# Kernel tuning notes

Hardware: AMD Instinct MI355X
Metric: run time of the kernel (lower is better)

The kernel has to match this reference:

```python
import jax, jax.numpy as jnp
import numpy as np

D_MODEL = 1024
N_HEADS = 16
D_HEAD = D_MODEL // N_HEADS
B, L = 4, 2048


def setup_inputs() -> dict:
    key = jax.random.key(0)
    ks = jax.random.split(key, 10)
    s = 1.0 / np.sqrt(D_MODEL)
    inp = {
        "x": jax.random.normal(ks[0], (B, L, D_MODEL), dtype=jnp.float32),
        "src_key_padding_mask": jax.random.randint(ks[1], (B, L), 0, 2) > 0,
        "wq": jax.random.uniform(ks[2], (D_MODEL, D_MODEL), jnp.float32, -s, s),
        "bq": jnp.zeros((D_MODEL,), jnp.float32),
        "wk": jax.random.uniform(ks[3], (D_MODEL, D_MODEL), jnp.float32, -s, s),
        "bk": jnp.zeros((D_MODEL,), jnp.float32),
        "wv": jax.random.uniform(ks[4], (D_MODEL, D_MODEL), jnp.float32, -s, s),
        "bv": jnp.zeros((D_MODEL,), jnp.float32),
        "wo": jax.random.uniform(ks[5], (D_MODEL, D_MODEL), jnp.float32, -s, s),
        "bo": jnp.zeros((D_MODEL,), jnp.float32),
    }
    return inp


def reference(x, src_key_padding_mask, wq, bq, wk, bk, wv, bv, wo, bo):
    # dropout is identity in eval mode
    Bx, Lx, D = x.shape
    H, dh = N_HEADS, D_HEAD

    def proj(w, b):
        # torch nn.Linear: y = x @ w.T + b
        y = jnp.einsum('bld,ed->ble', x, w) + b
        return y.reshape(Bx, Lx, H, dh).transpose(0, 2, 1, 3)  # (B,H,L,dh)

    q = proj(wq, bq)
    k = proj(wk, bk)
    v = proj(wv, bv)

    scores = jnp.einsum('bhqd,bhkd->bhqk', q, k) / jnp.sqrt(jnp.float32(dh))
    scores = jnp.where(src_key_padding_mask[:, None, None, :], jnp.float32(-1e9), scores)
    attn = jax.nn.softmax(scores, axis=-1)
    out = jnp.einsum('bhqk,bhkd->bhqd', attn, v)
    out = out.transpose(0, 2, 1, 3).reshape(Bx, Lx, D)
    out = jnp.einsum('bld,ed->ble', out, wo) + bo
    return out
```

## Files before the change

### kernel.cpp

```cpp
#include <hip/hip_runtime.h>


typedef __attribute__((ext_vector_type(8))) short short8;
typedef __attribute__((ext_vector_type(4))) float f32x4;
typedef __attribute__((ext_vector_type(4))) float floatx4;
typedef __attribute__((ext_vector_type(4))) int int4v;
typedef __attribute__((ext_vector_type(2))) unsigned int u32x2;

#define MFMA16(a, b, c) __builtin_amdgcn_mfma_f32_16x16x32_bf16((a), (b), (c), 0, 0, 0)

__device__ __forceinline__ short f2bf(float f) {
    unsigned u = __float_as_uint(f);
    u += 0x7FFF + ((u >> 16) & 1);
    return (short)(u >> 16);
}

__device__ __forceinline__ void gload_lds16(const short* g, short* l) {
    __builtin_amdgcn_global_load_lds(
        (const __attribute__((address_space(1))) void*)g,
        (__attribute__((address_space(3))) void*)l, 16, 0, 0);
}

__device__ __forceinline__ void cvt8(const float* __restrict__ src,
                                     short* __restrict__ dst, int i) {
    const f32x4* p = (const f32x4*)src + (size_t)i * 2;
    const f32x4 u0 = p[0];
    const f32x4 u1 = p[1];
    short8 s;
    s[0] = f2bf(u0[0]); s[1] = f2bf(u0[1]); s[2] = f2bf(u0[2]); s[3] = f2bf(u0[3]);
    s[4] = f2bf(u1[0]); s[5] = f2bf(u1[1]); s[6] = f2bf(u1[2]); s[7] = f2bf(u1[3]);
    ((short8*)dst)[i] = s;
}

__global__ __launch_bounds__(256) void cvt_kernel(
    const float* __restrict__ src, short* __restrict__ dst, int n8)
{
    const int i = blockIdx.x * 256 + threadIdx.x;
    if (i >= n8) return;
    cvt8(src, dst, i);
}

__global__ __launch_bounds__(256) void cvt3_kernel(
    const float* __restrict__ s0, const float* __restrict__ s1,
    const float* __restrict__ s2, short* __restrict__ d0,
    short* __restrict__ d1, short* __restrict__ d2)
{
    const int which = blockIdx.x >> 9;
    const int i = (blockIdx.x & 511) * 256 + threadIdx.x;
    const float* s = which == 0 ? s0 : which == 1 ? s1 : s2;
    short* d = which == 0 ? d0 : which == 1 ? d1 : d2;
    cvt8(s, d, i);
}

__global__ __launch_bounds__(256) void cvt2_kernel(
    const float* __restrict__ s0, short* __restrict__ d0,
    const float* __restrict__ s1, short* __restrict__ d1)
{
    if (blockIdx.x < 4096) {
        cvt8(s0, d0, blockIdx.x * 256 + threadIdx.x);
    } else {
        cvt8(s1, d1, (blockIdx.x - 4096) * 256 + threadIdx.x);
    }
}

__device__ __forceinline__ void gemm_body(
    const short* __restrict__ A, const short* __restrict__ W,
    const float* __restrict__ bias, void* __restrict__ out,
    int layout, int m0, int n0)
{
    __shared__ short As[128 * 32];
    __shared__ short Bs[128 * 32];

    const int t = threadIdx.x;
    const int wave = t >> 6, lane = t & 63;
    const int wm = (wave >> 1) * 64, wn = (wave & 1) * 64;
    const int l15 = lane & 15, quad = lane >> 4;

    const int r4 = lane >> 2;
    const int kc = (lane & 3) * 8;

    short* lA0 = &As[wave * 512 + lane * 8];
    short* lA1 = &As[2048 + wave * 512 + lane * 8];
    short* lB0 = &Bs[wave * 512 + lane * 8];
    short* lB1 = &Bs[2048 + wave * 512 + lane * 8];

    const short* gA0 = A + (size_t)(m0 + wave * 16 + r4) * 1024 + kc;
    const short* gA1 = gA0 + (size_t)64 * 1024;
    const short* gB0 = W + (size_t)(n0 + wave * 16 + r4) * 1024 + kc;
    const short* gB1 = gB0 + (size_t)64 * 1024;

    floatx4 acc[4][4];
#pragma unroll
    for (int i = 0; i < 4; i++)
#pragma unroll
        for (int j = 0; j < 4; j++) {
            acc[i][j][0] = 0.f; acc[i][j][1] = 0.f;
            acc[i][j][2] = 0.f; acc[i][j][3] = 0.f;
        }

    for (int kb = 0; kb < 1024; kb += 32) {
        gload_lds16(gA0 + kb, lA0);
        gload_lds16(gA1 + kb, lA1);
        gload_lds16(gB0 + kb, lB0);
        gload_lds16(gB1 + kb, lB1);
        __syncthreads();

        short8 af[4], bfr[4];
#pragma unroll
        for (int mi = 0; mi < 4; mi++)
            af[mi] = *(short8*)&As[(wm + mi * 16 + l15) * 32 + quad * 8];
#pragma unroll
        for (int ni = 0; ni < 4; ni++)
            bfr[ni] = *(short8*)&Bs[(wn + ni * 16 + l15) * 32 + quad * 8];
#pragma unroll
        for (int mi = 0; mi < 4; mi++)
#pragma unroll
            for (int ni = 0; ni < 4; ni++)
                acc[mi][ni] = MFMA16(af[mi], bfr[ni], acc[mi][ni]);

        __syncthreads();
    }

#pragma unroll
    for (int ni = 0; ni < 4; ni++) {
        const int gn = n0 + wn + ni * 16 + l15;
        const float bv = bias[gn];
#pragma unroll
        for (int mi = 0; mi < 4; mi++) {
#pragma unroll
            for (int r = 0; r < 4; r++) {
                const int gm = m0 + wm + mi * 16 + quad * 4 + r;
                const float v = acc[mi][ni][r] + bv;
                if (layout == 3) {
                    ((float*)out)[(size_t)gm * 1024 + gn] = v;
                } else {
                    const int b = gm >> 11, l = gm & 2047;
                    const int h = gn >> 6,  d = gn & 63;
                    size_t idx;
                    if (layout == 2)
                        idx = ((size_t)(b * 16 + h) * 64 + d) * 2048 + l;
                    else
                        idx = ((size_t)(b * 16 + h) * 2048 + l) * 64 + d;
                    ((short*)out)[idx] = f2bf(v);
                }
            }
        }
    }
}

__global__ __launch_bounds__(256, 3) void qkv_kernel(
    const short* __restrict__ Xb,
    const short* __restrict__ Wq, const short* __restrict__ Wk,
    const short* __restrict__ Wv,
    const float* __restrict__ bq, const float* __restrict__ bk,
    const float* __restrict__ bv,
    short* __restrict__ Qo, short* __restrict__ Ko, short* __restrict__ Vo)
{
    const int chunk = blockIdx.y >> 3;
    const int n0 = (blockIdx.y & 7) * 128;
    const short* W = chunk == 0 ? Wq : chunk == 1 ? Wk : Wv;
    const float* bs = chunk == 0 ? bq : chunk == 1 ? bk : bv;
    void* out = chunk == 0 ? (void*)Qo : chunk == 1 ? (void*)Ko : (void*)Vo;
    gemm_body(Xb, W, bs, out, chunk, blockIdx.x * 128, n0);
}

__global__ __launch_bounds__(256, 3) void gemm_kernel(
    const short* __restrict__ A, const short* __restrict__ W,
    const float* __restrict__ bias, void* __restrict__ out, int layout)
{
    gemm_body(A, W, bias, out, layout, blockIdx.x * 128, blockIdx.y * 128);
}

__global__ __launch_bounds__(256, 2) void attn_kernel(
    const short* __restrict__ Q, const short* __restrict__ Kc,
    const short* __restrict__ VT, const int* __restrict__ mask,
    float* __restrict__ O)
{
    __shared__ short Plds_all[4][4][16 * 72];

    const int blk = blockIdx.x;
    const int bh = blk & 63;
    const int qg = blk >> 6;
    const int b = bh >> 4, h = bh & 15;
    const int t = threadIdx.x;
    const int wave = t >> 6, lane = t & 63;
    const int l15 = lane & 15, quad = lane >> 4;

    const short* Qb = Q  + (size_t)bh * 2048 * 64;
    const short* Kb = Kc + (size_t)bh * 2048 * 64;
    const short* Vb = VT + (size_t)bh * 64 * 2048;
    const int* mrow = mask + b * 2048;

    const float SC = 0.125f * 1.44269504f;

    const int qbase = qg * 256 + wave * 64;

    short8 aq[4][2];
#pragma unroll
    for (int tt = 0; tt < 4; tt++) {
        const short* qp = Qb + (size_t)(qbase + tt * 16 + l15) * 64 + quad * 8;
        aq[tt][0] = *(const short8*)(qp);
        aq[tt][1] = *(const short8*)(qp + 32);
    }

    short8 vone;
#pragma unroll
    for (int j = 0; j < 8; j++) vone[j] = (short)0x3F80;

    floatx4 accO[4][5];
#pragma unroll
    for (int tt = 0; tt < 4; tt++)
#pragma unroll
        for (int ni = 0; ni < 5; ni++) {
            accO[tt][ni][0] = 0.f; accO[tt][ni][1] = 0.f;
            accO[tt][ni][2] = 0.f; accO[tt][ni][3] = 0.f;
        }

    for (int c0 = 0; c0 < 2048; c0 += 64) {
        short8 kreg[4][2];
#pragma unroll
        for (int g = 0; g < 4; g++) {
            const short* kp = Kb + (size_t)(c0 + g * 16 + l15) * 64 + quad * 8;
            kreg[g][0] = *(const short8*)(kp);
            kreg[g][1] = *(const short8*)(kp + 32);
        }
        f32x4 bias[4];
#pragma unroll
        for (int g = 0; g < 4; g++) {
            const int4v mv = *(const int4v*)&mrow[c0 + g * 16 + quad * 4];
#pragma unroll
            for (int r = 0; r < 4; r++) bias[g][r] = mv[r] ? -1e9f : 0.f;
        }
        short8 vreg[4][2];
#pragma unroll
        for (int ni = 0; ni < 4; ni++) {
            const short* vp = Vb + (size_t)(ni * 16 + l15) * 2048 + c0 + quad * 8;
            vreg[ni][0] = *(const short8*)(vp);
            vreg[ni][1] = *(const short8*)(vp + 32);
        }

#pragma unroll
        for (int tt = 0; tt < 4; tt++) {
            floatx4 s[4];
            __builtin_amdgcn_s_setprio(1);
#pragma unroll
            for (int g = 0; g < 4; g++) {
                floatx4 z = bias[g];
                z = MFMA16(kreg[g][0], aq[tt][0], z);
                s[g] = MFMA16(kreg[g][1], aq[tt][1], z);
            }
            __builtin_amdgcn_s_setprio(0);
            short* Pl = &Plds_all[wave][tt][0];
#pragma unroll
            for (int g = 0; g < 4; g++) {
                const float p0 = exp2f(s[g][0] * SC);
                const float p1 = exp2f(s[g][1] * SC);
                const float p2 = exp2f(s[g][2] * SC);
                const float p3 = exp2f(s[g][3] * SC);
                unsigned lo, hi;
                asm("v_cvt_pk_bf16_f32 %0, %1, %2" : "=v"(lo) : "v"(p0), "v"(p1));
                asm("v_cvt_pk_bf16_f32 %0, %1, %2" : "=v"(hi) : "v"(p2), "v"(p3));
                u32x2 w; w[0] = lo; w[1] = hi;
                *(u32x2*)&Pl[l15 * 72 + g * 16 + quad * 4] = w;
            }
        }

        asm volatile("s_waitcnt lgkmcnt(0)" ::: "memory");

#pragma unroll
        for (int tt = 0; tt < 4; tt++) {
            const short* Pl = &Plds_all[wave][tt][0];
            const short8 pa0 = *(const short8*)&Pl[l15 * 72 + quad * 8];
            const short8 pa1 = *(const short8*)&Pl[l15 * 72 + 32 + quad * 8];
            __builtin_amdgcn_s_setprio(1);
#pragma unroll
            for (int ni = 0; ni < 4; ni++) {
                accO[tt][ni] = MFMA16(pa0, vreg[ni][0], accO[tt][ni]);
                accO[tt][ni] = MFMA16(pa1, vreg[ni][1], accO[tt][ni]);
            }
            accO[tt][4] = MFMA16(pa0, vone, accO[tt][4]);
            accO[tt][4] = MFMA16(pa1, vone, accO[tt][4]);
            __builtin_amdgcn_s_setprio(0);
        }
    }

#pragma unroll
    for (int tt = 0; tt < 4; tt++) {
#pragma unroll
        for (int r = 0; r < 4; r++) {
            const float inv = 1.0f / fmaxf(accO[tt][4][r], 1e-30f);
            const int l = qbase + tt * 16 + quad * 4 + r;
#pragma unroll
            for (int ni = 0; ni < 4; ni++) {
                O[(size_t)(b * 2048 + l) * 1024 + h * 64 + ni * 16 + l15] =
                    accO[tt][ni][r] * inv;
            }
        }
    }
}

extern "C" void kernel_launch(void* const* d_in, const int* in_sizes, int n_in,
                              void* d_out, int out_size, void* d_ws, size_t ws_size,
                              hipStream_t stream)
{
    const float* x    = (const float*)d_in[0];
    const int*   mask = (const int*)d_in[1];
    const float* wq   = (const float*)d_in[2];
    const float* bq   = (const float*)d_in[3];
    const float* wk   = (const float*)d_in[4];
    const float* bk   = (const float*)d_in[5];
    const float* wv   = (const float*)d_in[6];
    const float* bv   = (const float*)d_in[7];
    const float* wo   = (const float*)d_in[8];
    const float* bo   = (const float*)d_in[9];
    float* out = (float*)d_out;

    short* Qbuf = (short*)d_ws;
    short* Kbuf = Qbuf + (size_t)8 * 1024 * 1024;
    short* Vt   = Kbuf + (size_t)8 * 1024 * 1024;

    short* Xb  = (short*)d_out;
    short* Wqb = Xb  + (size_t)8 * 1024 * 1024;
    short* Wkb = Wqb + (size_t)1024 * 1024;
    short* Wvb = Wkb + (size_t)1024 * 1024;

    dim3 block(256);

    cvt_kernel<<<dim3(4096), block, 0, stream>>>(x, Xb, 1024 * 1024);
    cvt3_kernel<<<dim3(1536), block, 0, stream>>>(wq, wk, wv, Wqb, Wkb, Wvb);

    qkv_kernel<<<dim3(64, 24), block, 0, stream>>>(
        Xb, Wqb, Wkb, Wvb, bq, bk, bv, Qbuf, Kbuf, Vt);

    attn_kernel<<<dim3(512), block, 0, stream>>>(Qbuf, Kbuf, Vt, mask, out);

    short* Ob  = Qbuf;
    short* Wob = Kbuf;
    cvt2_kernel<<<dim3(4608), block, 0, stream>>>(out, Ob, wo, Wob);

    gemm_kernel<<<dim3(64, 8), block, 0, stream>>>(Ob, Wob, bo, out, 3);
}
```

Baseline: 357.4 us.

## Use 256x256 tiled GEMMs with double-buffered LDS pipeline and tile swizzle

Replaces the 128x128 single-stage GEMM body with a 256x256 tile computed by 512 threads. It double-buffers K=64 slices in 128KB of dynamic LDS and interleaves global-to-LDS staging with MFMA phases, using explicit waitcnt, barriers and setprio. Block indices are remapped so neighbouring blocks share operand rows, which should help L2 reuse. The larger tile raises data reuse per load, but it leaves the output projection with only 128 blocks and the QKV GEMM with 384 blocks. That may underfill the CUs and give poor wave balance.

Measured after the change: 421.4 us. 17.9% more time.

```diff
diff --git a/kernel.cpp b/kernel.cpp
--- a/kernel.cpp
+++ b/kernel.cpp
@@ -63,73 +63,110 @@
     }
 }
 
-__device__ __forceinline__ void gemm_body(
+__device__ __forceinline__ void gemm256_body(
     const short* __restrict__ A, const short* __restrict__ W,
     const float* __restrict__ bias, void* __restrict__ out,
-    int layout, int m0, int n0)
-{
-    __shared__ short As[128 * 32];
-    __shared__ short Bs[128 * 32];
-
+    int layout, int m0, int n0, short* lds)
+{
     const int t = threadIdx.x;
     const int wave = t >> 6, lane = t & 63;
-    const int wm = (wave >> 1) * 64, wn = (wave & 1) * 64;
+    const int wr = wave >> 2, wc = wave & 3;
     const int l15 = lane & 15, quad = lane >> 4;
 
-    const int r4 = lane >> 2;
-    const int kc = (lane & 3) * 8;
-
-    short* lA0 = &As[wave * 512 + lane * 8];
-    short* lA1 = &As[2048 + wave * 512 + lane * 8];
-    short* lB0 = &Bs[wave * 512 + lane * 8];
-    short* lB1 = &Bs[2048 + wave * 512 + lane * 8];
-
-    const short* gA0 = A + (size_t)(m0 + wave * 16 + r4) * 1024 + kc;
-    const short* gA1 = gA0 + (size_t)64 * 1024;
-    const short* gB0 = W + (size_t)(n0 + wave * 16 + r4) * 1024 + kc;
-    const short* gB1 = gB0 + (size_t)64 * 1024;
-
-    floatx4 acc[4][4];
-#pragma unroll
-    for (int i = 0; i < 4; i++)
+    const int grow = t >> 3;
+    const int gcol = (t & 7) * 8;
+    const short* gA = A + (size_t)(m0 + grow) * 1024 + gcol;
+    const short* gB = W + (size_t)(n0 + grow) * 1024 + gcol;
+    short* ldst = lds + t * 8;
+
+    const int arow = (wr * 128 + l15) * 64 + quad * 8;
+    const int brow = 16384 + (wc * 64 + l15) * 64 + quad * 8;
+
+    f32x4 acc[8][4];
+#pragma unroll
+    for (int i = 0; i < 8; i++)
 #pragma unroll
         for (int j = 0; j < 4; j++) {
             acc[i][j][0] = 0.f; acc[i][j][1] = 0.f;
             acc[i][j][2] = 0.f; acc[i][j][3] = 0.f;
         }
 
-    for (int kb = 0; kb < 1024; kb += 32) {
-        gload_lds16(gA0 + kb, lA0);
-        gload_lds16(gA1 + kb, lA1);
-        gload_lds16(gB0 + kb, lB0);
-        gload_lds16(gB1 + kb, lB1);
-        __syncthreads();
-
-        short8 af[4], bfr[4];
-#pragma unroll
-        for (int mi = 0; mi < 4; mi++)
-            af[mi] = *(short8*)&As[(wm + mi * 16 + l15) * 32 + quad * 8];
-#pragma unroll
-        for (int ni = 0; ni < 4; ni++)
-            bfr[ni] = *(short8*)&Bs[(wn + ni * 16 + l15) * 32 + quad * 8];
-#pragma unroll
-        for (int mi = 0; mi < 4; mi++)
-#pragma unroll
-            for (int ni = 0; ni < 4; ni++)
-                acc[mi][ni] = MFMA16(af[mi], bfr[ni], acc[mi][ni]);
-
-        __syncthreads();
-    }
+#define STAGE(T, h, isA, p) do {                                              \
+    const short* g_ = ((isA) ? gA : gB) + (size_t)((h) * 128) * 1024          \
+                      + (size_t)(T) * 64;                                     \
+    short* l_ = ldst + (p) * 32768 + ((isA) ? 0 : 16384) + (h) * 8192;        \
+    gload_lds16(g_, l_);                                                      \
+    gload_lds16(g_ + 64 * 1024, l_ + 4096);                                   \
+} while (0)
+
+    short8 bf[4][2];
+
+#define PHASE(p, q, T_st, h_st, isA_st, p_st, do_vm) do {                     \
+    short8 af[2][2];                                                          \
+    _Pragma("unroll")                                                         \
+    for (int j = 0; j < 2; j++)                                               \
+        _Pragma("unroll")                                                     \
+        for (int ks = 0; ks < 2; ks++)                                        \
+            af[j][ks] = *(const short8*)                                      \
+                &lds[(p) * 32768 + arow + ((q) * 2 + j) * 1024 + ks * 32];    \
+    if ((q) == 0) {                                                           \
+        _Pragma("unroll")                                                     \
+        for (int ni = 0; ni < 4; ni++)                                        \
+            _Pragma("unroll")                                                 \
+            for (int ks = 0; ks < 2; ks++)                                    \
+                bf[ni][ks] = *(const short8*)                                 \
+                    &lds[(p) * 32768 + brow + ni * 1024 + ks * 32];           \
+    }                                                                         \
+    STAGE(T_st, h_st, isA_st, p_st);                                          \
+    if (do_vm) asm volatile("s_waitcnt vmcnt(4)");                            \
+    __builtin_amdgcn_s_barrier();                                             \
+    asm volatile("s_waitcnt lgkmcnt(0)");                                     \
+    __builtin_amdgcn_sched_barrier(0);                                        \
+    __builtin_amdgcn_s_setprio(1);                                            \
+    _Pragma("unroll")                                                         \
+    for (int j = 0; j < 2; j++)                                               \
+        _Pragma("unroll")                                                     \
+        for (int ni = 0; ni < 4; ni++) {                                      \
+            acc[(q) * 2 + j][ni] =                                            \
+                MFMA16(af[j][0], bf[ni][0], acc[(q) * 2 + j][ni]);            \
+            acc[(q) * 2 + j][ni] =                                            \
+                MFMA16(af[j][1], bf[ni][1], acc[(q) * 2 + j][ni]);            \
+        }                                                                     \
+    __builtin_amdgcn_s_setprio(0);                                            \
+    __builtin_amdgcn_s_barrier();                                             \
+} while (0)
+
+    STAGE(0, 0, false, 0); STAGE(0, 1, false, 0);
+    STAGE(0, 0, true,  0); STAGE(0, 1, true,  0);
+    STAGE(1, 0, false, 1); STAGE(1, 1, false, 1);
+    asm volatile("s_waitcnt vmcnt(4)");
+    __builtin_amdgcn_s_barrier();
+
+    for (int i = 0; i < 8; i++) {
+        const int t1 = 2 * i + 1;
+        const int n2 = (2 * i + 2) & 15;
+        const int n3 = (2 * i + 3) & 15;
+        PHASE(0, 0, t1, 0, true,  1, false);
+        PHASE(0, 1, t1, 1, true,  1, false);
+        PHASE(0, 2, n2, 0, false, 0, false);
+        PHASE(0, 3, n2, 1, false, 0, true);
+        PHASE(1, 0, n2, 0, true,  0, false);
+        PHASE(1, 1, n2, 1, true,  0, false);
+        PHASE(1, 2, n3, 0, false, 1, false);
+        PHASE(1, 3, n3, 1, false, 1, true);
+    }
+#undef PHASE
+#undef STAGE
 
 #pragma unroll
     for (int ni = 0; ni < 4; ni++) {
-        const int gn = n0 + wn + ni * 16 + l15;
+        const int gn = n0 + wc * 64 + ni * 16 + l15;
         const float bv = bias[gn];
 #pragma unroll
-        for (int mi = 0; mi < 4; mi++) {
+        for (int mi = 0; mi < 8; mi++) {
 #pragma unroll
             for (int r = 0; r < 4; r++) {
-                const int gm = m0 + wm + mi * 16 + quad * 4 + r;
+                const int gm = m0 + wr * 128 + mi * 16 + quad * 4 + r;
                 const float v = acc[mi][ni][r] + bv;
                 if (layout == 3) {
                     ((float*)out)[(size_t)gm * 1024 + gn] = v;
@@ -148,7 +185,7 @@
     }
 }
 
-__global__ __launch_bounds__(256, 3) void qkv_kernel(
+__global__ __launch_bounds__(512, 2) void qkv_kernel(
     const short* __restrict__ Xb,
     const short* __restrict__ Wq, const short* __restrict__ Wk,
     const short* __restrict__ Wv,
@@ -156,19 +193,27 @@
     const float* __restrict__ bv,
     short* __restrict__ Qo, short* __restrict__ Ko, short* __restrict__ Vo)
 {
-    const int chunk = blockIdx.y >> 3;
-    const int n0 = (blockIdx.y & 7) * 128;
+    extern __shared__ short lds[];
+    const int id = blockIdx.y * 32 + blockIdx.x;
+    const int nid = (id & 7) * 48 + (id >> 3);
+    const int bx = nid & 31, by = nid >> 5;
+    const int chunk = by >> 2;
+    const int n0 = (by & 3) * 256;
     const short* W = chunk == 0 ? Wq : chunk == 1 ? Wk : Wv;
     const float* bs = chunk == 0 ? bq : chunk == 1 ? bk : bv;
     void* out = chunk == 0 ? (void*)Qo : chunk == 1 ? (void*)Ko : (void*)Vo;
-    gemm_body(Xb, W, bs, out, chunk, blockIdx.x * 128, n0);
-}
-
-__global__ __launch_bounds__(256, 3) void gemm_kernel(
+    gemm256_body(Xb, W, bs, out, chunk, bx * 256, n0, lds);
+}
+
+__global__ __launch_bounds__(512, 2) void gemm_kernel(
     const short* __restrict__ A, const short* __restrict__ W,
     const float* __restrict__ bias, void* __restrict__ out, int layout)
 {
-    gemm_body(A, W, bias, out, layout, blockIdx.x * 128, blockIdx.y * 128);
+    extern __shared__ short lds[];
+    const int id = blockIdx.y * 32 + blockIdx.x;
+    const int nid = (id & 7) * 16 + (id >> 3);
+    const int bx = nid & 31, by = nid >> 5;
+    gemm256_body(A, W, bias, out, layout, bx * 256, by * 256, lds);
 }
 
 __global__ __launch_bounds__(256, 2) void attn_kernel(
@@ -315,6 +360,15 @@
     const float* bo   = (const float*)d_in[9];
     float* out = (float*)d_out;
 
+    static bool lds_init = false;
+    if (!lds_init) {
+        (void)hipFuncSetAttribute((const void*)qkv_kernel,
+            hipFuncAttributeMaxDynamicSharedMemorySize, 131072);
+        (void)hipFuncSetAttribute((const void*)gemm_kernel,
+            hipFuncAttributeMaxDynamicSharedMemorySize, 131072);
+        lds_init = true;
+    }
+
     short* Qbuf = (short*)d_ws;
     short* Kbuf = Qbuf + (size_t)8 * 1024 * 1024;
     short* Vt   = Kbuf + (size_t)8 * 1024 * 1024;
@@ -329,7 +383,7 @@
     cvt_kernel<<<dim3(4096), block, 0, stream>>>(x, Xb, 1024 * 1024);
     cvt3_kernel<<<dim3(1536), block, 0, stream>>>(wq, wk, wv, Wqb, Wkb, Wvb);
 
-    qkv_kernel<<<dim3(64, 24), block, 0, stream>>>(
+    qkv_kernel<<<dim3(32, 12), dim3(512), 131072, stream>>>(
         Xb, Wqb, Wkb, Wvb, bq, bk, bv, Qbuf, Kbuf, Vt);
 
     attn_kernel<<<dim3(512), block, 0, stream>>>(Qbuf, Kbuf, Vt, mask, out);
@@ -338,5 +392,5 @@
     short* Wob = Kbuf;
     cvt2_kernel<<<dim3(4608), block, 0, stream>>>(out, Ob, wo, Wob);
 
-    gemm_kernel<<<dim3(64, 8), block, 0, stream>>>(Ob, Wob, bo, out, 3);
-}
+    gemm_kernel<<<dim3(32, 4), dim3(512), 131072, stream>>>(Ob, Wob, bo, out, 3);
+}
```
